# Performance work log

Hardware: AMD Instinct MI355X
Metric: run time of the kernel (lower is better)

Reference implementation:

```python
import jax, jax.numpy as jnp
import numpy as np

B, T, D, H = 8, 4096, 1024, 16
DK = D // H
CHUNK = 64
E, TOPK, MULT, CAPF = 8, 2, 4, 1.25
HID = D * MULT
N = B * T
CAPACITY = int(CAPF * (N / E))  # 5120


def setup_inputs() -> dict:
    key = jax.random.key(0)
    ks = jax.random.split(key, 16)
    s = 0.02
    r = lambda k, shape: jax.random.normal(k, shape, jnp.float32) * s
    return {
        "x": jax.random.normal(ks[0], (B, T, D), jnp.float32),
        "norm1_scale": jnp.ones((D,), jnp.float32),
        "norm2_scale": jnp.ones((D,), jnp.float32),
        "Wq": r(ks[1], (D, D)), "bq": jnp.zeros((D,), jnp.float32),
        "Wk": r(ks[2], (D, D)), "bk": jnp.zeros((D,), jnp.float32),
        "Wv": r(ks[3], (D, D)), "bv": jnp.zeros((D,), jnp.float32),
        "Wg": r(ks[4], (D, D)), "bg": jnp.zeros((D,), jnp.float32),
        "Wo": r(ks[5], (D, D)), "bo": jnp.zeros((D,), jnp.float32),
        "router_W": r(ks[6], (D, E)), "router_b": jnp.zeros((E,), jnp.float32),
        "W1": r(ks[7], (E, D, HID)), "b1": jnp.zeros((E, HID), jnp.float32),
        "W2": r(ks[8], (E, HID, D)), "b2": jnp.zeros((E, D), jnp.float32),
    }


def rmsnorm(x, scale):
    # torch: x / (||x|| / sqrt(d)) * scale == x * rsqrt(mean(x^2)) * scale (no eps)
    return x / jnp.sqrt(jnp.mean(x * x, axis=-1, keepdims=True)) * scale


def apply_rope(x):
    # x: (B, H, T, DK); non-interleaved half-rotation as in source
    half = x.shape[-1] // 2
    t = x.shape[2]
    inv = 1.0 / (10000.0 ** (jnp.arange(half, dtype=jnp.float32) / half))
    ang = jnp.arange(t, dtype=jnp.float32)[:, None] * inv[None, :]  # (T, half)
    sin, cos = jnp.sin(ang)[None, None], jnp.cos(ang)[None, None]
    x1, x2 = x[..., :half], x[..., half:]
    return jnp.concatenate([x1 * cos - x2 * sin, x1 * sin + x2 * cos], axis=-1)


def phi(x):
    return jax.nn.elu(x) + 1.0


def attention(x, Wq, bq, Wk, bk, Wv, bv, Wg, bg, Wo, bo):
    b, t, c = x.shape
    heads = lambda y: y.reshape(b, t, H, DK).transpose(0, 2, 1, 3)  # (B,H,T,DK)
    q = phi(apply_rope(heads(x @ Wq + bq)))
    k = phi(apply_rope(heads(x @ Wk + bk)))
    v = heads(x @ Wv + bv)
    g = heads(jax.nn.sigmoid(x @ Wg + bg))
    nc = t // CHUNK
    to_chunks = lambda y: y.reshape(b, H, nc, CHUNK, DK).transpose(2, 0, 1, 3, 4)
    qs, ks_, vs, gs = map(to_chunks, (q, k, v, g))  # (nc,B,H,chunk,DK)
    S0 = jnp.zeros((b, H, DK, DK), x.dtype)
    Z0 = jnp.zeros((b, H, DK), x.dtype)

    def step(carry, inp):
        S, Z = carry
        qc, kc, vc, gc = inp
        S = S + jnp.einsum('bhtd,bhte->bhde', kc, vc)
        Z = Z + kc.sum(axis=2)
        num = jnp.einsum('bhtd,bhde->bhte', qc, S)
        den = jnp.einsum('bhtd,bhd->bht', qc, Z)[..., None] + 1e-6
        return (S, Z), gc * (num / den)

    _, outs = jax.lax.scan(step, (S0, Z0), (qs, ks_, vs, gs))  # (nc,B,H,chunk,DK)
    out = outs.transpose(1, 2, 0, 3, 4).reshape(b, H, t, DK)
    out = out.transpose(0, 2, 1, 3).reshape(b, t, c)
    return out @ Wo + bo


def moe(x, router_W, router_b, W1, b1, W2, b2):
    b, t, c = x.shape
    n = b * t
    xf = x.reshape(n, c)
    probs = jax.nn.softmax(xf @ router_W + router_b, axis=-1)
    topk_probs, topk_idx = jax.lax.top_k(probs, TOPK)
    topk_probs = topk_probs / topk_probs.sum(axis=-1, keepdims=True)
    out = jnp.zeros_like(xf)
    load = []
    for eid in range(E):  # fixed small expert loop (matches source structure)
        mask = (topk_idx == eid).reshape(-1)  # row-major == torch.where order
        idx = jnp.nonzero(mask, size=CAPACITY, fill_value=n * TOPK)[0]
        valid = idx < n * TOPK
        idxc = jnp.minimum(idx, n * TOPK - 1)
        tok, choice = idxc // TOPK, idxc % TOPK
        h = jax.nn.gelu(xf[tok] @ W1[eid] + b1[eid], approximate=False) @ W2[eid] + b2[eid]
        gate = jnp.where(valid, topk_probs[tok, choice], 0.0)
        out = out.at[tok].add(gate[:, None] * h)  # invalid slots have gate==0
        load.append(jnp.minimum(mask.sum(), CAPACITY).astype(xf.dtype))
    load = jnp.stack(load)
    importance = probs.sum(axis=0)
    importance = importance / importance.sum()
    load = load / load.sum()
    aux = (importance * load).sum() * (E ** 2)
    return out.reshape(b, t, c), aux


def reference(x, norm1_scale, norm2_scale, Wq, bq, Wk, bk, Wv, bv, Wg, bg, Wo, bo,
              router_W, router_b, W1, b1, W2, b2):
    x = x + attention(rmsnorm(x, norm1_scale), Wq, bq, Wk, bk, Wv, bv, Wg, bg, Wo, bo)
    moe_out, aux = moe(rmsnorm(x, norm2_scale), router_W, router_b, W1, b1, W2, b2)
    return (x + moe_out, aux)
```

## Files before the change

### kernel.cpp

```cpp
#include <hip/hip_runtime.h>
#include <hip/hip_bf16.h>

#define NTOK 32768
#define TSEQ 4096
#define DM   1024
#define NHEAD 16
#define NEXP 8
#define CAPE 5120
#define HIDN 4096
#define GTOK 8192
#define KSPL 5120

#ifndef __has_builtin
#define __has_builtin(x) 0
#endif
#if __has_builtin(__builtin_amdgcn_global_load_lds)
#define HAVE_GLOAD 1
#else
#define HAVE_GLOAD 0
#endif

typedef __attribute__((ext_vector_type(8))) short bf16x8;
typedef __attribute__((ext_vector_type(4))) float f32x4;

__device__ __forceinline__ float phi_f(float v) { return v > 0.f ? v + 1.f : expf(v); }

__device__ __forceinline__ unsigned short f2bf_bits(float f) {
    __hip_bfloat16 h = __float2bfloat16(f);
    union { __hip_bfloat16 h; unsigned short s; } u;
    u.h = h;
    return u.s;
}
__device__ __forceinline__ float bf_to_f(unsigned short s) {
    unsigned int u = ((unsigned int)s) << 16;
    union { unsigned int u; float f; } w; w.u = u;
    return w.f;
}

__global__ void k_ws_flag(float* out, float v) { if (threadIdx.x == 0) out[0] = v; }

__global__ void k_zero(int* p, int n) {
    int i = blockIdx.x * 256 + threadIdx.x;
    if (i < n) p[i] = 0;
}

__global__ __launch_bounds__(256) void k_rope_table(float* __restrict__ ct, float* __restrict__ st)
{
    const int idx = blockIdx.x * 256 + threadIdx.x;
    const int t = idx >> 5, j = idx & 31;
    const float inv = (float)(1.0 / pow(10000.0, (double)j / 32.0));
    float sn, cn;
    sincosf((float)t * inv, &sn, &cn);
    ct[idx] = cn; st[idx] = sn;
}

struct WPack { const float* W[5]; };
__global__ __launch_bounds__(256) void k_build_wstack(WPack P, __hip_bfloat16* __restrict__ BTbase)
{
    __shared__ float t_[32][33];
    const int z = blockIdx.z;
    const float* Wm = P.W[z];
    __hip_bfloat16* BT = BTbase + (size_t)z * DM * KSPL;
    const int n0 = blockIdx.x * 32, k0 = blockIdx.y * 32;
    const int c = threadIdx.x & 31, r0 = (threadIdx.x >> 5);
#pragma unroll
    for (int i = 0; i < 4; ++i) { int r = r0 + i * 8; t_[r][c] = Wm[(size_t)(k0 + r) * DM + n0 + c]; }
    __syncthreads();
#pragma unroll
    for (int i = 0; i < 4; ++i) {
        int r = r0 + i * 8;
        float val = t_[c][r];
        unsigned short b0 = f2bf_bits(val);
        float res = val - bf_to_f(b0);
        unsigned short b1 = f2bf_bits(res);
        __hip_bfloat16 h0, h1;
        union { __hip_bfloat16 h; unsigned short s; } u0, u1;
        u0.s = b0; u1.s = b1; h0 = u0.h; h1 = u1.h;
        const size_t nrow = (size_t)(n0 + r) * KSPL + (k0 + c);
        BT[nrow]            = h0;
        BT[nrow + 1024]     = h0;
        BT[nrow + 2048]     = h0;
        BT[nrow + 3072]     = h1;
        BT[nrow + 4096]     = h1;
    }
}

template<bool NORM>
__global__ __launch_bounds__(256) void k_rms_split(const float* __restrict__ X,
                                                   const float* __restrict__ nscale,
                                                   __hip_bfloat16* __restrict__ Xs)
{
    const int row = blockIdx.x;
    const int tid = threadIdx.x;
    const float* xr = X + (size_t)row * DM;
    float4 v = ((const float4*)xr)[tid];
    float r = 1.f;
    if (NORM) {
        float s = v.x * v.x + v.y * v.y + v.z * v.z + v.w * v.w;
        for (int off = 32; off; off >>= 1) s += __shfl_xor(s, off);
        __shared__ float redw[4];
        __shared__ float rbc;
        if ((tid & 63) == 0) redw[tid >> 6] = s;
        __syncthreads();
        if (tid == 0) {
            float tot = redw[0] + redw[1] + redw[2] + redw[3];
            rbc = (float)(1.0 / sqrt((double)tot * (1.0 / 1024.0)));
        }
        __syncthreads();
        r = rbc;
    }
    float c[4] = {v.x, v.y, v.z, v.w};
    if (NORM) {
        float4 ns = ((const float4*)nscale)[tid];
        c[0] *= r * ns.x; c[1] *= r * ns.y; c[2] *= r * ns.z; c[3] *= r * ns.w;
    }
    ushort4 p0, p1, p2;
    unsigned short* q0 = (unsigned short*)&p0;
    unsigned short* q1 = (unsigned short*)&p1;
    unsigned short* q2 = (unsigned short*)&p2;
#pragma unroll
    for (int i = 0; i < 4; ++i) {
        float x = c[i];
        unsigned short b0 = f2bf_bits(x);
        float r1 = x - bf_to_f(b0);
        unsigned short b1 = f2bf_bits(r1);
        float r2 = r1 - bf_to_f(b1);
        unsigned short b2 = f2bf_bits(r2);
        q0[i] = b0; q1[i] = b1; q2[i] = b2;
    }
    __hip_bfloat16* base = Xs + (size_t)row * 3072;
    ((ushort4*)(base))[tid] = p0;
    ((ushort4*)(base + 1024))[tid] = p1;
    ((ushort4*)(base + 2048))[tid] = p2;
}

__global__ __launch_bounds__(256) void k_rmsnorm_stats(const float* __restrict__ X,
                                                       float* __restrict__ rn,
                                                       const float* __restrict__ nscale,
                                                       __hip_bfloat16* __restrict__ xbf)
{
    const int row = blockIdx.x;
    const int tid = threadIdx.x;
    const float* xr = X + (size_t)row * DM;
    float4 v = ((const float4*)xr)[tid];
    float s = v.x * v.x + v.y * v.y + v.z * v.z + v.w * v.w;
    for (int off = 32; off; off >>= 1) s += __shfl_xor(s, off);
    __shared__ float redw[4];
    __shared__ float rbc;
    if ((tid & 63) == 0) redw[tid >> 6] = s;
    __syncthreads();
    if (tid == 0) {
        float tot = redw[0] + redw[1] + redw[2] + redw[3];
        float r = (float)(1.0 / sqrt((double)tot * (1.0 / 1024.0)));
        rn[row] = r; rbc = r;
    }
    __syncthreads();
    float r = rbc;
    float4 ns = ((const float4*)nscale)[tid];
    ushort4 o;
    o.x = f2bf_bits(v.x * r * ns.x);
    o.y = f2bf_bits(v.y * r * ns.y);
    o.z = f2bf_bits(v.z * r * ns.z);
    o.w = f2bf_bits(v.w * r * ns.w);
    ((ushort4*)(xbf + (size_t)row * DM))[tid] = o;
}

#if HAVE_GLOAD
__device__ __forceinline__ void gload16(const __hip_bfloat16* g, __hip_bfloat16* l)
{
    __builtin_amdgcn_global_load_lds((const __attribute__((address_space(1))) unsigned int*)g,
                                     (__attribute__((address_space(3))) unsigned int*)l, 16, 0, 0);
}
#endif


struct ProjPack {
    const __hip_bfloat16* BT[4];
    const float* bias[4];
    float* C[4];
};

template<int NMAT, bool RESID>
__global__ __launch_bounds__(256) void k_gemm_proj(const __hip_bfloat16* __restrict__ A,
                                                   ProjPack P,
                                                   const float* __restrict__ resid)
{
    const int z = (NMAT == 4) ? blockIdx.z : 0;
    const __hip_bfloat16* BT = P.BT[z];
    const float* bias = P.bias[z];
    float* C = P.C[z];
    const int m0 = blockIdx.y * 128;
    const int n0 = blockIdx.x * 128;
    const int tid = threadIdx.x;
    __shared__ alignas(16) __hip_bfloat16 As[2][128 * 32];
    __shared__ alignas(16) __hip_bfloat16 Bs[2][128 * 32];

    const int lane = tid & 63, wv = tid >> 6;
    const int lr = lane & 15, lgp = lane >> 4;
    const int wm = (wv >> 1) * 64, wn = (wv & 1) * 64;

#if HAVE_GLOAD
    const int rA0 = wv * 32 + (lane >> 2), rA1 = rA0 + 16;
    const int ch = lane & 3;
    const __hip_bfloat16* srcA0 = A + (size_t)(m0 + rA0) * 3072 + ((ch ^ (rA0 & 3)) * 8);
    const __hip_bfloat16* srcA1 = A + (size_t)(m0 + rA1) * 3072 + ((ch ^ (rA1 & 3)) * 8);
    const __hip_bfloat16* srcB0 = BT + (size_t)(n0 + rA0) * KSPL + ((ch ^ (rA0 & 3)) * 8);
    const __hip_bfloat16* srcB1 = BT + (size_t)(n0 + rA1) * KSPL + ((ch ^ (rA1 & 3)) * 8);
    const int ldsO0 = (wv * 32) * 32;
    const int ldsO1 = (wv * 32 + 16) * 32;
#else
    const int ar = tid >> 1, ac0 = (tid & 1) * 2;
    const __hip_bfloat16* Arow = A + (size_t)(m0 + ar) * 3072;
    const __hip_bfloat16* Brow = BT + (size_t)(n0 + ar) * KSPL;
#endif

    f32x4 acc[4][4];
#pragma unroll
    for (int i = 0; i < 4; ++i)
#pragma unroll
        for (int j = 0; j < 4; ++j) acc[i][j] = (f32x4){0.f, 0.f, 0.f, 0.f};

    int a_off[4], b_off[4];
#pragma unroll
    for (int i = 0; i < 4; ++i) {
        int mrow = wm + i * 16 + lr;
        a_off[i] = mrow * 32 + ((lgp ^ (mrow & 3)) * 8);
        int nrow = wn + i * 16 + lr;
        b_off[i] = nrow * 32 + ((lgp ^ (nrow & 3)) * 8);
    }

#if HAVE_GLOAD
    gload16(srcA0, &As[0][ldsO0]);
    gload16(srcA1, &As[0][ldsO1]);
    gload16(srcB0, &Bs[0][ldsO0]);
    gload16(srcB1, &Bs[0][ldsO1]);
#else
    {
        uint4 av0 = *(const uint4*)(Arow + ac0 * 8);
        uint4 av1 = *(const uint4*)(Arow + ac0 * 8 + 8);
        uint4 bv0 = *(const uint4*)(Brow + ac0 * 8);
        uint4 bv1 = *(const uint4*)(Brow + ac0 * 8 + 8);
        *(uint4*)(&As[0][0] + ar * 32 + ((ac0    ) ^ (ar & 3)) * 8) = av0;
        *(uint4*)(&As[0][0] + ar * 32 + ((ac0 + 1) ^ (ar & 3)) * 8) = av1;
        *(uint4*)(&Bs[0][0] + ar * 32 + ((ac0    ) ^ (ar & 3)) * 8) = bv0;
        *(uint4*)(&Bs[0][0] + ar * 32 + ((ac0 + 1) ^ (ar & 3)) * 8) = bv1;
    }
#endif
    __syncthreads();

    int cur = 0;
    for (int k0 = 0; k0 < KSPL; k0 += 32) {
        if (k0 + 32 < KSPL) {
            const int kn = k0 + 32;
            const int acoln = (kn < 3072) ? kn : (kn - 3072);
#if HAVE_GLOAD
            gload16(srcA0 + acoln, &As[cur ^ 1][ldsO0]);
            gload16(srcA1 + acoln, &As[cur ^ 1][ldsO1]);
            gload16(srcB0 + kn, &Bs[cur ^ 1][ldsO0]);
            gload16(srcB1 + kn, &Bs[cur ^ 1][ldsO1]);
#else
            uint4 av0 = *(const uint4*)(Arow + acoln + ac0 * 8);
            uint4 av1 = *(const uint4*)(Arow + acoln + ac0 * 8 + 8);
            uint4 bv0 = *(const uint4*)(Brow + kn + ac0 * 8);
            uint4 bv1 = *(const uint4*)(Brow + kn + ac0 * 8 + 8);
            *(uint4*)(&As[cur ^ 1][0] + ar * 32 + ((ac0    ) ^ (ar & 3)) * 8) = av0;
            *(uint4*)(&As[cur ^ 1][0] + ar * 32 + ((ac0 + 1) ^ (ar & 3)) * 8) = av1;
            *(uint4*)(&Bs[cur ^ 1][0] + ar * 32 + ((ac0    ) ^ (ar & 3)) * 8) = bv0;
            *(uint4*)(&Bs[cur ^ 1][0] + ar * 32 + ((ac0 + 1) ^ (ar & 3)) * 8) = bv1;
#endif
        }
        bf16x8 af[4], bfr[4];
#pragma unroll
        for (int i = 0; i < 4; ++i) af[i] = *(const bf16x8*)(&As[cur][0] + a_off[i]);
#pragma unroll
        for (int j = 0; j < 4; ++j) bfr[j] = *(const bf16x8*)(&Bs[cur][0] + b_off[j]);
#pragma unroll
        for (int i = 0; i < 4; ++i)
#pragma unroll
            for (int j = 0; j < 4; ++j)
                acc[i][j] = __builtin_amdgcn_mfma_f32_16x16x32_bf16(af[i], bfr[j], acc[i][j], 0, 0, 0);
        __syncthreads();
        cur ^= 1;
    }

#pragma unroll
    for (int i = 0; i < 4; ++i)
#pragma unroll
        for (int j = 0; j < 4; ++j) {
            const int col = n0 + wn + j * 16 + lr;
            const float bval = bias[col];
#pragma unroll
            for (int r = 0; r < 4; ++r) {
                const int rloc = wm + i * 16 + lgp * 4 + r;
                float v = acc[i][j][r] + bval;
                if (RESID) v += resid[(size_t)(m0 + rloc) * DM + col];
                C[(size_t)(m0 + rloc) * DM + col] = v;
            }
        }
}

template<int MODE>
__global__ __launch_bounds__(256) void k_gemm_bf16(const __hip_bfloat16* __restrict__ A,
                                                   const __hip_bfloat16* __restrict__ BT,
                                                   const float* __restrict__ bias,
                                                   __hip_bfloat16* __restrict__ Hout,
                                                   float* __restrict__ Fout,
                                                   const int* __restrict__ tokslot,
                                                   const float* __restrict__ gateslot,
                                                   int K, int Nout, int e0)
{
    const int le = blockIdx.z;
    const int e = e0 + le;
    const int m0 = blockIdx.y * 128;
    const int n0 = blockIdx.x * 128;
    const int tid = threadIdx.x;
    __shared__ alignas(16) __hip_bfloat16 As[2][128 * 32];
    __shared__ alignas(16) __hip_bfloat16 Bs[2][128 * 32];
    __shared__ int s_tok[128];
    __shared__ float s_gate[128];
    if (tid < 128) {
        s_tok[tid] = tokslot[e * CAPE + m0 + tid];
        s_gate[tid] = gateslot[e * CAPE + m0 + tid];
    }
    __syncthreads();

    const int lane = tid & 63, wv = tid >> 6;
    const int lr = lane & 15, lgp = lane >> 4;
    const int wm = (wv >> 1) * 64, wn = (wv & 1) * 64;

#if HAVE_GLOAD
    const int rA0 = wv * 32 + (lane >> 2), rA1 = rA0 + 16;
    const int ch = lane & 3;
    const __hip_bfloat16 *srcA0, *srcA1;
    if (MODE == 0) {
        srcA0 = A + (size_t)s_tok[rA0] * K + ((ch ^ (rA0 & 3)) * 8);
        srcA1 = A + (size_t)s_tok[rA1] * K + ((ch ^ (rA1 & 3)) * 8);
    } else {
        srcA0 = A + ((size_t)le * CAPE + m0 + rA0) * K + ((ch ^ (rA0 & 3)) * 8);
        srcA1 = A + ((size_t)le * CAPE + m0 + rA1) * K + ((ch ^ (rA1 & 3)) * 8);
    }
    const __hip_bfloat16* srcB0 = BT + ((size_t)e * Nout + n0 + rA0) * K + ((ch ^ (rA0 & 3)) * 8);
    const __hip_bfloat16* srcB1 = BT + ((size_t)e * Nout + n0 + rA1) * K + ((ch ^ (rA1 & 3)) * 8);
    const int ldsO0 = (wv * 32) * 32;
    const int ldsO1 = (wv * 32 + 16) * 32;
#else
    const int ar = tid >> 1, ac0 = (tid & 1) * 2;
    const __hip_bfloat16* Arow;
    if (MODE == 0) Arow = A + (size_t)s_tok[ar] * K;
    else           Arow = A + ((size_t)le * CAPE + m0 + ar) * K;
    const __hip_bfloat16* Brow = BT + ((size_t)e * Nout + n0 + ar) * K;
#endif

    f32x4 acc[4][4];
#pragma unroll
    for (int i = 0; i < 4; ++i)
#pragma unroll
        for (int j = 0; j < 4; ++j) acc[i][j] = (f32x4){0.f, 0.f, 0.f, 0.f};

    int a_off[4], b_off[4];
#pragma unroll
    for (int i = 0; i < 4; ++i) {
        int mrow = wm + i * 16 + lr;
        a_off[i] = mrow * 32 + ((lgp ^ (mrow & 3)) * 8);
        int nrow = wn + i * 16 + lr;
        b_off[i] = nrow * 32 + ((lgp ^ (nrow & 3)) * 8);
    }

#if HAVE_GLOAD
    gload16(srcA0, &As[0][ldsO0]);
    gload16(srcA1, &As[0][ldsO1]);
    gload16(srcB0, &Bs[0][ldsO0]);
    gload16(srcB1, &Bs[0][ldsO1]);
#else
    {
        uint4 av0 = *(const uint4*)(Arow + ac0 * 8);
        uint4 av1 = *(const uint4*)(Arow + ac0 * 8 + 8);
        uint4 bv0 = *(const uint4*)(Brow + ac0 * 8);
        uint4 bv1 = *(const uint4*)(Brow + ac0 * 8 + 8);
        *(uint4*)(&As[0][0] + ar * 32 + ((ac0    ) ^ (ar & 3)) * 8) = av0;
        *(uint4*)(&As[0][0] + ar * 32 + ((ac0 + 1) ^ (ar & 3)) * 8) = av1;
        *(uint4*)(&Bs[0][0] + ar * 32 + ((ac0    ) ^ (ar & 3)) * 8) = bv0;
        *(uint4*)(&Bs[0][0] + ar * 32 + ((ac0 + 1) ^ (ar & 3)) * 8) = bv1;
    }
#endif
    __syncthreads();

    int cur = 0;
    for (int k0 = 0; k0 < K; k0 += 32) {
        if (k0 + 32 < K) {
            const int kn = k0 + 32;
#if HAVE_GLOAD
            gload16(srcA0 + kn, &As[cur ^ 1][ldsO0]);
            gload16(srcA1 + kn, &As[cur ^ 1][ldsO1]);
            gload16(srcB0 + kn, &Bs[cur ^ 1][ldsO0]);
            gload16(srcB1 + kn, &Bs[cur ^ 1][ldsO1]);
#else
            uint4 av0 = *(const uint4*)(Arow + kn + ac0 * 8);
            uint4 av1 = *(const uint4*)(Arow + kn + ac0 * 8 + 8);
            uint4 bv0 = *(const uint4*)(Brow + kn + ac0 * 8);
            uint4 bv1 = *(const uint4*)(Brow + kn + ac0 * 8 + 8);
            *(uint4*)(&As[cur ^ 1][0] + ar * 32 + ((ac0    ) ^ (ar & 3)) * 8) = av0;
            *(uint4*)(&As[cur ^ 1][0] + ar * 32 + ((ac0 + 1) ^ (ar & 3)) * 8) = av1;
            *(uint4*)(&Bs[cur ^ 1][0] + ar * 32 + ((ac0    ) ^ (ar & 3)) * 8) = bv0;
            *(uint4*)(&Bs[cur ^ 1][0] + ar * 32 + ((ac0 + 1) ^ (ar & 3)) * 8) = bv1;
#endif
        }
        bf16x8 af[4], bfr[4];
#pragma unroll
        for (int i = 0; i < 4; ++i) af[i] = *(const bf16x8*)(&As[cur][0] + a_off[i]);
#pragma unroll
        for (int j = 0; j < 4; ++j) bfr[j] = *(const bf16x8*)(&Bs[cur][0] + b_off[j]);
#pragma unroll
        for (int i = 0; i < 4; ++i)
#pragma unroll
            for (int j = 0; j < 4; ++j)
                acc[i][j] = __builtin_amdgcn_mfma_f32_16x16x32_bf16(af[i], bfr[j], acc[i][j], 0, 0, 0);
        __syncthreads();
        cur ^= 1;
    }

#pragma unroll
    for (int i = 0; i < 4; ++i)
#pragma unroll
        for (int j = 0; j < 4; ++j) {
            const int col = n0 + wn + j * 16 + lr;
            const float bval = bias[(size_t)e * Nout + col];
#pragma unroll
            for (int r = 0; r < 4; ++r) {
                const int rloc = wm + i * 16 + lgp * 4 + r;
                float v = acc[i][j][r] + bval;
                if (MODE == 0) {
                    v = 0.5f * v * (1.f + erff(v * 0.70710678118654752f));
                    Hout[((size_t)le * CAPE + m0 + rloc) * Nout + col] = __float2bfloat16(v);
                } else {
                    const float g = s_gate[rloc];
                    if (g != 0.f) atomicAdd(&Fout[(size_t)s_tok[rloc] * DM + col], v * g);
                }
            }
        }
}

__global__ __launch_bounds__(256) void k_scan_kv(float* KS, float* Vz,
                                                 const float* __restrict__ ct,
                                                 const float* __restrict__ st)
{
    const int c = blockIdx.x, bh = blockIdx.y;
    const int h = bh & 15, b = bh >> 4;
    const int tid = threadIdx.x;
    __shared__ float ks[64][68];
    __shared__ float vs[64][68];
    const size_t rowbase = ((size_t)b * TSEQ + c * 64) * DM + h * 64;
#pragma unroll
    for (int p = 0; p < 8; ++p) {
        int idx = p * 256 + tid;
        int t = idx >> 5, j = idx & 31;
        const size_t base = rowbase + (size_t)t * DM + j;
        float cn = ct[(c * 64 + t) * 32 + j];
        float sn = st[(c * 64 + t) * 32 + j];
        float k1 = KS[base], k2 = KS[base + 32];
        ks[t][j]      = phi_f(k1 * cn - k2 * sn);
        ks[t][j + 32] = phi_f(k1 * sn + k2 * cn);
    }
#pragma unroll
    for (int p = 0; p < 4; ++p) {
        int idx = p * 256 + tid;
        int t = idx >> 4, e4 = (idx & 15) * 4;
        *(float4*)&vs[t][e4] = *(const float4*)&Vz[rowbase + (size_t)t * DM + e4];
    }
    __syncthreads();
    const int e = tid & 63, dg = tid >> 6;
    float acc[16] = {};
    for (int t = 0; t < 64; ++t) {
        float vv = vs[t][e];
#pragma unroll
        for (int qq = 0; qq < 4; ++qq) {
            float4 kq = *(const float4*)&ks[t][dg * 16 + qq * 4];
            acc[qq * 4 + 0] = fmaf(kq.x, vv, acc[qq * 4 + 0]);
            acc[qq * 4 + 1] = fmaf(kq.y, vv, acc[qq * 4 + 1]);
            acc[qq * 4 + 2] = fmaf(kq.z, vv, acc[qq * 4 + 2]);
            acc[qq * 4 + 3] = fmaf(kq.w, vv, acc[qq * 4 + 3]);
        }
    }
#pragma unroll
    for (int i = 0; i < 16; ++i) {
        int d = dg * 16 + i;
        KS[rowbase + (size_t)d * DM + e] = acc[i];
    }
    if (tid < 64) {
        float z = 0.f;
        for (int t = 0; t < 64; ++t) z += ks[t][tid];
        Vz[rowbase + tid] = z;
    }
}

__global__ __launch_bounds__(256) void k_scan_prefix(float* S)
{
    const int sg = blockIdx.x, bh = blockIdx.y;
    const int h = bh & 15, b = bh >> 4;
    const int idx = sg * 256 + threadIdx.x;
    const int d = idx >> 6, e = idx & 63;
    const size_t base = (size_t)b * TSEQ * DM + h * 64 + (size_t)d * DM + e;
    float acc = 0.f;
    for (int c = 0; c < 64; ++c) {
        size_t p = base + (size_t)c * 64 * DM;
        acc += S[p];
        S[p] = acc;
    }
}

__global__ void k_zprefix(float* Vz)
{
    const int bh = blockIdx.x;
    const int h = bh & 15, b = bh >> 4;
    const int d = threadIdx.x;
    const size_t base = (size_t)b * TSEQ * DM + h * 64 + d;
    float acc = 0.f;
    for (int c = 0; c < 64; ++c) {
        size_t p = base + (size_t)c * 64 * DM;
        acc += Vz[p];
        Vz[p] = acc;
    }
}

__global__ __launch_bounds__(256) void k_scan_out(const float* __restrict__ Q,
                                                  const float* __restrict__ S,
                                                  const float* __restrict__ Zv,
                                                  const float* __restrict__ G,
                                                  __hip_bfloat16* __restrict__ Xs,
                                                  const float* __restrict__ ct,
                                                  const float* __restrict__ st)
{
    const int c = blockIdx.x, bh = blockIdx.y;
    const int h = bh & 15, b = bh >> 4;
    const int tid = threadIdx.x;
    __shared__ float qs[64][69];
    __shared__ float Ss[64][68];
    __shared__ float den[64], Zl[64];
    const size_t rowbase = ((size_t)b * TSEQ + c * 64) * DM + h * 64;
#pragma unroll
    for (int p = 0; p < 8; ++p) {
        int idx = p * 256 + tid;
        int t = idx >> 5, j = idx & 31;
        const size_t base = rowbase + (size_t)t * DM + j;
        float cn = ct[(c * 64 + t) * 32 + j];
        float sn = st[(c * 64 + t) * 32 + j];
        float q1 = Q[base], q2 = Q[base + 32];
        qs[t][j]      = phi_f(q1 * cn - q2 * sn);
        qs[t][j + 32] = phi_f(q1 * sn + q2 * cn);
    }
#pragma unroll
    for (int p = 0; p < 4; ++p) {
        int idx = p * 256 + tid;
        int d = idx >> 4, e4 = (idx & 15) * 4;
        *(float4*)&Ss[d][e4] = *(const float4*)&S[rowbase + (size_t)d * DM + e4];
    }
    const int e = tid & 63, tg = tid >> 6;
    float greg[16];
#pragma unroll
    for (int i = 0; i < 16; ++i)
        greg[i] = G[rowbase + (size_t)(tg * 16 + i) * DM + e];
    if (tid < 64) Zl[tid] = Zv[rowbase + tid];
    __syncthreads();
    if (tid < 64) {
        float dd = 0.f;
        for (int d = 0; d < 64; ++d) dd += qs[tid][d] * Zl[d];
        den[tid] = dd + 1e-6f;
    }
    __syncthreads();
    float acc[16] = {};
    for (int d = 0; d < 64; ++d) {
        float sv = Ss[d][e];
#pragma unroll
        for (int i = 0; i < 16; ++i)
            acc[i] = fmaf(qs[tg * 16 + i][d], sv, acc[i]);
    }
    unsigned short* Xu = (unsigned short*)Xs;
#pragma unroll
    for (int i = 0; i < 16; ++i) {
        int t = tg * 16 + i;
        float g = 1.f / (1.f + expf(-greg[i]));
        float o = g * acc[i] / den[t];
        unsigned short b0 = f2bf_bits(o);
        float r1 = o - bf_to_f(b0);
        unsigned short b1 = f2bf_bits(r1);
        float r2 = r1 - bf_to_f(b1);
        unsigned short b2 = f2bf_bits(r2);
        const size_t xb = (size_t)(b * TSEQ + c * 64 + t) * 3072 + h * 64 + e;
        Xu[xb] = b0;
        Xu[xb + 1024] = b1;
        Xu[xb + 2048] = b2;
    }
}

__global__ __launch_bounds__(256) void k_router(const float* __restrict__ X2,
                                                const float* __restrict__ rn2,
                                                const float* __restrict__ ns2,
                                                const float* __restrict__ rW,
                                                const float* __restrict__ rb,
                                                int* __restrict__ route_e,
                                                float* __restrict__ route_g,
                                                float* __restrict__ probs)
{
    const int tok = blockIdx.x * 4 + (threadIdx.x >> 6);
    const int lane = threadIdx.x & 63;
    const float* xr = X2 + (size_t)tok * DM;
    const float rn = rn2[tok];
    float lg[8] = {};
    for (int d = lane; d < DM; d += 64) {
        float xv = xr[d] * rn * ns2[d];
        const float4* w4 = (const float4*)(rW + (size_t)d * 8);
        float4 w0 = w4[0], w1 = w4[1];
        lg[0] += xv * w0.x; lg[1] += xv * w0.y; lg[2] += xv * w0.z; lg[3] += xv * w0.w;
        lg[4] += xv * w1.x; lg[5] += xv * w1.y; lg[6] += xv * w1.z; lg[7] += xv * w1.w;
    }
#pragma unroll
    for (int e = 0; e < 8; ++e)
        for (int off = 32; off; off >>= 1) lg[e] += __shfl_xor(lg[e], off);
    if (lane == 0) {
        float pe[8]; float mx = -1e30f, s = 0.f;
#pragma unroll
        for (int e = 0; e < 8; ++e) { lg[e] += rb[e]; mx = fmaxf(mx, lg[e]); }
#pragma unroll
        for (int e = 0; e < 8; ++e) { pe[e] = expf(lg[e] - mx); s += pe[e]; }
#pragma unroll
        for (int e = 0; e < 8; ++e) { pe[e] /= s; probs[(size_t)tok * 8 + e] = pe[e]; }
        int i1 = 0; float p1 = pe[0];
#pragma unroll
        for (int e = 1; e < 8; ++e) if (pe[e] > p1) { p1 = pe[e]; i1 = e; }
        int i2 = -1; float p2 = -1.f;
#pragma unroll
        for (int e = 0; e < 8; ++e) if (e != i1 && pe[e] > p2) { p2 = pe[e]; i2 = e; }
        const float gsum = p1 + p2;
        route_e[tok * 2] = i1; route_e[tok * 2 + 1] = i2;
        route_g[tok * 2] = p1 / gsum; route_g[tok * 2 + 1] = p2 / gsum;
    }
}

__global__ __launch_bounds__(256) void k_count(const int* __restrict__ route_e, int* __restrict__ bcnt)
{
    __shared__ int c[8];
    const int tid = threadIdx.x;
    if (tid < 8) c[tid] = 0;
    __syncthreads();
    atomicAdd(&c[route_e[blockIdx.x * 256 + tid]], 1);
    __syncthreads();
    if (tid < 8) bcnt[blockIdx.x * 8 + tid] = c[tid];
}

__global__ void k_scan_blocks(const int* __restrict__ bcnt, int* __restrict__ bbase, int* __restrict__ ctot)
{
    const int e = threadIdx.x;
    if (e < 8) {
        int run = 0;
        for (int b = 0; b < 256; ++b) { bbase[b * 8 + e] = run; run += bcnt[b * 8 + e]; }
        ctot[e] = run;
    }
}

__global__ __launch_bounds__(256) void k_place(const int* __restrict__ route_e,
                                               const float* __restrict__ route_g,
                                               const int* __restrict__ bbase,
                                               int* __restrict__ tokslot,
                                               float* __restrict__ gateslot)
{
    const int tid = threadIdx.x;
    const int a = blockIdx.x * 256 + tid;
    const int e = route_e[a];
    __shared__ int se[256];
    se[tid] = e;
    __syncthreads();
    int rank = 0;
    for (int j = 0; j < tid; ++j) rank += (se[j] == e) ? 1 : 0;
    const int slot = bbase[blockIdx.x * 8 + e] + rank;
    if (slot < CAPE) {
        tokslot[e * CAPE + slot] = a >> 1;
        gateslot[e * CAPE + slot] = route_g[a];
    }
}

__global__ __launch_bounds__(256) void k_aux(const float* __restrict__ probs,
                                             const int* __restrict__ ctot,
                                             float* __restrict__ out_aux)
{
    const int tid = threadIdx.x;
    float part[8] = {};
    for (int i = tid; i < NTOK; i += 256) {
        const float* p = probs + (size_t)i * 8;
#pragma unroll
        for (int e = 0; e < 8; ++e) part[e] += p[e];
    }
    __shared__ float red[256];
    __shared__ float accs[8];
    for (int e = 0; e < 8; ++e) {
        red[tid] = part[e];
        __syncthreads();
        for (int s = 128; s; s >>= 1) { if (tid < s) red[tid] += red[tid + s]; __syncthreads(); }
        if (tid == 0) accs[e] = red[0];
        __syncthreads();
    }
    if (tid == 0) {
        float isum = 0.f, lsum = 0.f, l[8];
        for (int e = 0; e < 8; ++e) isum += accs[e];
        for (int e = 0; e < 8; ++e) { l[e] = fminf((float)ctot[e], (float)CAPE); lsum += l[e]; }
        float aux = 0.f;
        for (int e = 0; e < 8; ++e) aux += (accs[e] / isum) * (l[e] / lsum);
        out_aux[0] = aux * 64.f;
    }
}

__global__ void k_transpose_bf16(const float* __restrict__ src, __hip_bfloat16* __restrict__ dst,
                                 int K_, int N_)
{
    __shared__ float t_[32][33];
    const int z = blockIdx.z;
    const float* s = src + (size_t)z * K_ * N_;
    __hip_bfloat16* d = dst + (size_t)z * K_ * N_;
    const int n0 = blockIdx.x * 32, k0 = blockIdx.y * 32;
    const int c = threadIdx.x, r0 = threadIdx.y;
#pragma unroll
    for (int i = 0; i < 4; ++i) { int r = r0 + i * 8; t_[r][c] = s[(size_t)(k0 + r) * N_ + n0 + c]; }
    __syncthreads();
#pragma unroll
    for (int i = 0; i < 4; ++i) { int r = r0 + i * 8; d[(size_t)(n0 + r) * K_ + k0 + c] = __float2bfloat16(t_[c][r]); }
}

extern "C" void kernel_launch(void* const* d_in, const int* in_sizes, int n_in,
                              void* d_out, int out_size, void* d_ws, size_t ws_size,
                              hipStream_t stream)
{
    (void)in_sizes; (void)n_in; (void)out_size;
    const float* x   = (const float*)d_in[0];
    const float* ns1 = (const float*)d_in[1];
    const float* ns2 = (const float*)d_in[2];
    const float* Wq  = (const float*)d_in[3];
    const float* bq  = (const float*)d_in[4];
    const float* Wk  = (const float*)d_in[5];
    const float* bk  = (const float*)d_in[6];
    const float* Wv  = (const float*)d_in[7];
    const float* bv  = (const float*)d_in[8];
    const float* Wg  = (const float*)d_in[9];
    const float* bg  = (const float*)d_in[10];
    const float* Wo  = (const float*)d_in[11];
    const float* bo  = (const float*)d_in[12];
    const float* rW  = (const float*)d_in[13];
    const float* rb  = (const float*)d_in[14];
    const float* W1  = (const float*)d_in[15];
    const float* b1  = (const float*)d_in[16];
    const float* W2  = (const float*)d_in[17];
    const float* b2  = (const float*)d_in[18];
    float* out = (float*)d_out;
    char* wsb = (char*)d_ws;

    constexpr size_t MiB = 1024ull * 1024ull;
    constexpr size_t R = (size_t)NTOK * DM * 4;
    constexpr size_t TAIL = 3 * R;
    constexpr size_t OFF_RN1  = TAIL;
    constexpr size_t OFF_RN2  = OFF_RN1 + (size_t)NTOK * 4;
    constexpr size_t OFF_PROB = OFF_RN2 + (size_t)NTOK * 4;
    constexpr size_t OFF_RE   = OFF_PROB + (size_t)NTOK * 8 * 4;
    constexpr size_t OFF_RG   = OFF_RE + (size_t)NTOK * 2 * 4;
    constexpr size_t OFF_BCNT = OFF_RG + (size_t)NTOK * 2 * 4;
    constexpr size_t OFF_BBASE= OFF_BCNT + 256 * 8 * 4;
    constexpr size_t OFF_CTOT = OFF_BBASE + 256 * 8 * 4;
    constexpr size_t OFF_TOK  = OFF_CTOT + 4096;
    constexpr size_t OFF_GATE = OFF_TOK + (size_t)NEXP * CAPE * 4;
    constexpr size_t REQUIRED = OFF_GATE + (size_t)NEXP * CAPE * 4;

    if (ws_size < REQUIRED) {
        k_ws_flag<<<1, 64, 0, stream>>>(out, (float)(ws_size >> 20));
        return;
    }

    __hip_bfloat16* xn2bf = (__hip_bfloat16*)(wsb);
    __hip_bfloat16* WST   = (__hip_bfloat16*)(wsb + 64 * MiB);
    __hip_bfloat16* Xs    = (__hip_bfloat16*)(wsb + 114 * MiB);
    float* qg = (float*)(wsb + 162 * MiB);
    float* kg = (float*)(wsb + 194 * MiB);
    float* gg = (float*)(wsb + 226 * MiB);
    __hip_bfloat16* W1T  = (__hip_bfloat16*)(wsb + 64 * MiB);
    __hip_bfloat16* W2T  = (__hip_bfloat16*)(wsb + 128 * MiB);
    __hip_bfloat16* Hbuf = (__hip_bfloat16*)(wsb + 192 * MiB);

    float* rn2 = (float*)(wsb + OFF_RN2);
    float* probs = (float*)(wsb + OFF_PROB);
    float* rope_ct = (float*)(wsb + OFF_PROB);
    float* rope_st = (float*)(wsb + OFF_PROB + (size_t)TSEQ * 32 * 4);
    int*   route_e = (int*)(wsb + OFF_RE);
    float* route_g = (float*)(wsb + OFF_RG);
    int*   bcnt  = (int*)(wsb + OFF_BCNT);
    int*   bbase = (int*)(wsb + OFF_BBASE);
    int*   ctot  = (int*)(wsb + OFF_CTOT);
    int*   tokslot  = (int*)(wsb + OFF_TOK);
    float* gateslot = (float*)(wsb + OFF_GATE);

    k_rope_table<<<512, 256, 0, stream>>>(rope_ct, rope_st);
    {
        WPack WP; WP.W[0] = Wq; WP.W[1] = Wk; WP.W[2] = Wg; WP.W[3] = Wv; WP.W[4] = Wo;
        k_build_wstack<<<dim3(32, 32, 5), 256, 0, stream>>>(WP, WST);
    }

    for (int gi = 0; gi < 4; ++gi) {
        const size_t tok0 = (size_t)gi * GTOK;
        const float* xg = x + tok0 * DM;
        float* vg = out + tok0 * DM;

        k_rms_split<true><<<GTOK, 256, 0, stream>>>(xg, ns1, Xs);

        ProjPack P;
        P.BT[0] = WST;                     P.bias[0] = bq; P.C[0] = qg;
        P.BT[1] = WST + (size_t)DM * KSPL; P.bias[1] = bk; P.C[1] = kg;
        P.BT[2] = WST + 2ull * DM * KSPL;  P.bias[2] = bg; P.C[2] = gg;
        P.BT[3] = WST + 3ull * DM * KSPL;  P.bias[3] = bv; P.C[3] = vg;
        k_gemm_proj<4, false><<<dim3(8, GTOK / 128, 4), 256, 0, stream>>>(Xs, P, nullptr);

        k_scan_kv<<<dim3(64, 32), 256, 0, stream>>>(kg, vg, rope_ct, rope_st);
        k_scan_prefix<<<dim3(16, 32), 256, 0, stream>>>(kg);
        k_zprefix<<<32, 64, 0, stream>>>(vg);
        k_scan_out<<<dim3(64, 32), 256, 0, stream>>>(qg, kg, vg, gg, Xs, rope_ct, rope_st);

        ProjPack P2;
        P2.BT[0] = WST + 4ull * DM * KSPL; P2.bias[0] = bo; P2.C[0] = vg;
        P2.BT[1] = P2.BT[2] = P2.BT[3] = P2.BT[0];
        P2.bias[1] = P2.bias[2] = P2.bias[3] = bo;
        P2.C[1] = P2.C[2] = P2.C[3] = vg;
        k_gemm_proj<1, true><<<dim3(8, GTOK / 128, 1), 256, 0, stream>>>(Xs, P2, xg);

        k_rmsnorm_stats<<<GTOK, 256, 0, stream>>>(vg, rn2 + tok0, ns2, xn2bf + tok0 * DM);
    }

    k_router<<<NTOK / 4, 256, 0, stream>>>(out, rn2, ns2, rW, rb, route_e, route_g, probs);

    k_count<<<256, 256, 0, stream>>>(route_e, bcnt);
    k_scan_blocks<<<1, 64, 0, stream>>>(bcnt, bbase, ctot);
    k_zero<<<(NEXP * CAPE * 2 + 255) / 256, 256, 0, stream>>>(tokslot, NEXP * CAPE * 2);
    k_place<<<256, 256, 0, stream>>>(route_e, route_g, bbase, tokslot, gateslot);

    k_aux<<<1, 256, 0, stream>>>(probs, ctot, out + (size_t)NTOK * DM);

    k_transpose_bf16<<<dim3(HIDN / 32, DM / 32, NEXP), dim3(32, 8), 0, stream>>>(W1, W1T, DM, HIDN);
    k_transpose_bf16<<<dim3(DM / 32, HIDN / 32, NEXP), dim3(32, 8), 0, stream>>>(W2, W2T, HIDN, DM);

    for (int g = 0; g < 3; ++g) {
        const int e0 = g * 3;
        const int ecnt = (g == 2) ? 2 : 3;
        k_gemm_bf16<0><<<dim3(HIDN / 128, CAPE / 128, ecnt), 256, 0, stream>>>(
            xn2bf, W1T, b1, Hbuf, nullptr, tokslot, gateslot, DM, HIDN, e0);
        k_gemm_bf16<1><<<dim3(DM / 128, CAPE / 128, ecnt), 256, 0, stream>>>(
            Hbuf, W2T, b2, nullptr, out, tokslot, gateslot, HIDN, DM, e0);
    }
}
```

Before: 4.610 ms.

## Use triple-buffered LDS pipeline with explicit vmcnt waits in GEMM kernels

The projection and expert GEMM kernels move from a double-buffered LDS scheme to a three-stage ring. Three tiles are prefetched through global_load_lds, and the loop waits with explicit s_waitcnt vmcnt counts and raw s_barrier calls instead of __syncthreads. This lets the loads for tile t+3 overlap the MFMA work on tile t and takes the blanket vmcnt(0) out of each iteration. In exchange LDS use per block rises by half, which may lower occupancy, and correctness now depends on the hand-written wait counts matching the number of outstanding loads.

```diff
diff --git a/kernel.cpp b/kernel.cpp
--- a/kernel.cpp
+++ b/kernel.cpp
@@ -22,6 +22,11 @@
 
 typedef __attribute__((ext_vector_type(8))) short bf16x8;
 typedef __attribute__((ext_vector_type(4))) float f32x4;
+
+#define WAITCNT8() asm volatile("s_waitcnt vmcnt(8)" ::: "memory")
+#define WAITCNT4() asm volatile("s_waitcnt vmcnt(4)" ::: "memory")
+#define WAITCNT0() asm volatile("s_waitcnt vmcnt(0)" ::: "memory")
+#define RAWBAR()   do { asm volatile("" ::: "memory"); __builtin_amdgcn_s_barrier(); asm volatile("" ::: "memory"); } while (0)
 
 __device__ __forceinline__ float phi_f(float v) { return v > 0.f ? v + 1.f : expf(v); }
 
@@ -192,12 +197,29 @@
     const int m0 = blockIdx.y * 128;
     const int n0 = blockIdx.x * 128;
     const int tid = threadIdx.x;
-    __shared__ alignas(16) __hip_bfloat16 As[2][128 * 32];
-    __shared__ alignas(16) __hip_bfloat16 Bs[2][128 * 32];
+    __shared__ alignas(16) __hip_bfloat16 As[3][128 * 32];
+    __shared__ alignas(16) __hip_bfloat16 Bs[3][128 * 32];
 
     const int lane = tid & 63, wv = tid >> 6;
     const int lr = lane & 15, lgp = lane >> 4;
     const int wm = (wv >> 1) * 64, wn = (wv & 1) * 64;
+
+    f32x4 acc[4][4];
+#pragma unroll
+    for (int i = 0; i < 4; ++i)
+#pragma unroll
+        for (int j = 0; j < 4; ++j) acc[i][j] = (f32x4){0.f, 0.f, 0.f, 0.f};
+
+    int a_off[4], b_off[4];
+#pragma unroll
+    for (int i = 0; i < 4; ++i) {
+        int mrow = wm + i * 16 + lr;
+        a_off[i] = mrow * 32 + ((lgp ^ (mrow & 3)) * 8);
+        int nrow = wn + i * 16 + lr;
+        b_off[i] = nrow * 32 + ((lgp ^ (nrow & 3)) * 8);
+    }
+
+    constexpr int T = KSPL / 32;
 
 #if HAVE_GLOAD
     const int rA0 = wv * 32 + (lane >> 2), rA1 = rA0 + 16;
@@ -208,80 +230,68 @@
     const __hip_bfloat16* srcB1 = BT + (size_t)(n0 + rA1) * KSPL + ((ch ^ (rA1 & 3)) * 8);
     const int ldsO0 = (wv * 32) * 32;
     const int ldsO1 = (wv * 32 + 16) * 32;
+
+    auto STAGE = [&](int tile, int buf) {
+        const int kb = tile * 32;
+        const int acol = (kb < 3072) ? kb : (kb - 3072);
+        gload16(srcA0 + acol, &As[buf][ldsO0]);
+        gload16(srcA1 + acol, &As[buf][ldsO1]);
+        gload16(srcB0 + kb,  &Bs[buf][ldsO0]);
+        gload16(srcB1 + kb,  &Bs[buf][ldsO1]);
+    };
+
+    STAGE(0, 0); STAGE(1, 1); STAGE(2, 2);
+    int buf = 0;
+    for (int t = 0; t < T; ++t) {
+        if (t <= T - 3)      { WAITCNT8(); }
+        else if (t == T - 2) { WAITCNT4(); }
+        else                 { WAITCNT0(); }
+        RAWBAR();
+        bf16x8 af[4], bfr[4];
+#pragma unroll
+        for (int i = 0; i < 4; ++i) af[i] = *(const bf16x8*)(&As[buf][0] + a_off[i]);
+#pragma unroll
+        for (int j = 0; j < 4; ++j) bfr[j] = *(const bf16x8*)(&Bs[buf][0] + b_off[j]);
+#pragma unroll
+        for (int i = 0; i < 4; ++i)
+#pragma unroll
+            for (int j = 0; j < 4; ++j)
+                acc[i][j] = __builtin_amdgcn_mfma_f32_16x16x32_bf16(af[i], bfr[j], acc[i][j], 0, 0, 0);
+        if (t + 3 < T) {
+            RAWBAR();
+            STAGE(t + 3, buf);
+        }
+        buf = (buf == 2) ? 0 : buf + 1;
+    }
 #else
     const int ar = tid >> 1, ac0 = (tid & 1) * 2;
     const __hip_bfloat16* Arow = A + (size_t)(m0 + ar) * 3072;
     const __hip_bfloat16* Brow = BT + (size_t)(n0 + ar) * KSPL;
-#endif
-
-    f32x4 acc[4][4];
-#pragma unroll
-    for (int i = 0; i < 4; ++i)
-#pragma unroll
-        for (int j = 0; j < 4; ++j) acc[i][j] = (f32x4){0.f, 0.f, 0.f, 0.f};
-
-    int a_off[4], b_off[4];
-#pragma unroll
-    for (int i = 0; i < 4; ++i) {
-        int mrow = wm + i * 16 + lr;
-        a_off[i] = mrow * 32 + ((lgp ^ (mrow & 3)) * 8);
-        int nrow = wn + i * 16 + lr;
-        b_off[i] = nrow * 32 + ((lgp ^ (nrow & 3)) * 8);
-    }
-
-#if HAVE_GLOAD
-    gload16(srcA0, &As[0][ldsO0]);
-    gload16(srcA1, &As[0][ldsO1]);
-    gload16(srcB0, &Bs[0][ldsO0]);
-    gload16(srcB1, &Bs[0][ldsO1]);
-#else
-    {
-        uint4 av0 = *(const uint4*)(Arow + ac0 * 8);
-        uint4 av1 = *(const uint4*)(Arow + ac0 * 8 + 8);
-        uint4 bv0 = *(const uint4*)(Brow + ac0 * 8);
-        uint4 bv1 = *(const uint4*)(Brow + ac0 * 8 + 8);
+    for (int t = 0; t < T; ++t) {
+        const int kb = t * 32;
+        const int acol = (kb < 3072) ? kb : (kb - 3072);
+        __syncthreads();
+        uint4 av0 = *(const uint4*)(Arow + acol + ac0 * 8);
+        uint4 av1 = *(const uint4*)(Arow + acol + ac0 * 8 + 8);
+        uint4 bv0 = *(const uint4*)(Brow + kb + ac0 * 8);
+        uint4 bv1 = *(const uint4*)(Brow + kb + ac0 * 8 + 8);
         *(uint4*)(&As[0][0] + ar * 32 + ((ac0    ) ^ (ar & 3)) * 8) = av0;
         *(uint4*)(&As[0][0] + ar * 32 + ((ac0 + 1) ^ (ar & 3)) * 8) = av1;
         *(uint4*)(&Bs[0][0] + ar * 32 + ((ac0    ) ^ (ar & 3)) * 8) = bv0;
         *(uint4*)(&Bs[0][0] + ar * 32 + ((ac0 + 1) ^ (ar & 3)) * 8) = bv1;
-    }
-#endif
-    __syncthreads();
-
-    int cur = 0;
-    for (int k0 = 0; k0 < KSPL; k0 += 32) {
-        if (k0 + 32 < KSPL) {
-            const int kn = k0 + 32;
-            const int acoln = (kn < 3072) ? kn : (kn - 3072);
-#if HAVE_GLOAD
-            gload16(srcA0 + acoln, &As[cur ^ 1][ldsO0]);
-            gload16(srcA1 + acoln, &As[cur ^ 1][ldsO1]);
-            gload16(srcB0 + kn, &Bs[cur ^ 1][ldsO0]);
-            gload16(srcB1 + kn, &Bs[cur ^ 1][ldsO1]);
-#else
-            uint4 av0 = *(const uint4*)(Arow + acoln + ac0 * 8);
-            uint4 av1 = *(const uint4*)(Arow + acoln + ac0 * 8 + 8);
-            uint4 bv0 = *(const uint4*)(Brow + kn + ac0 * 8);
-            uint4 bv1 = *(const uint4*)(Brow + kn + ac0 * 8 + 8);
-            *(uint4*)(&As[cur ^ 1][0] + ar * 32 + ((ac0    ) ^ (ar & 3)) * 8) = av0;
-            *(uint4*)(&As[cur ^ 1][0] + ar * 32 + ((ac0 + 1) ^ (ar & 3)) * 8) = av1;
-            *(uint4*)(&Bs[cur ^ 1][0] + ar * 32 + ((ac0    ) ^ (ar & 3)) * 8) = bv0;
-            *(uint4*)(&Bs[cur ^ 1][0] + ar * 32 + ((ac0 + 1) ^ (ar & 3)) * 8) = bv1;
-#endif
-        }
+        __syncthreads();
         bf16x8 af[4], bfr[4];
 #pragma unroll
-        for (int i = 0; i < 4; ++i) af[i] = *(const bf16x8*)(&As[cur][0] + a_off[i]);
-#pragma unroll
-        for (int j = 0; j < 4; ++j) bfr[j] = *(const bf16x8*)(&Bs[cur][0] + b_off[j]);
+        for (int i = 0; i < 4; ++i) af[i] = *(const bf16x8*)(&As[0][0] + a_off[i]);
+#pragma unroll
+        for (int j = 0; j < 4; ++j) bfr[j] = *(const bf16x8*)(&Bs[0][0] + b_off[j]);
 #pragma unroll
         for (int i = 0; i < 4; ++i)
 #pragma unroll
             for (int j = 0; j < 4; ++j)
                 acc[i][j] = __builtin_amdgcn_mfma_f32_16x16x32_bf16(af[i], bfr[j], acc[i][j], 0, 0, 0);
-        __syncthreads();
-        cur ^= 1;
-    }
+    }
+#endif
 
 #pragma unroll
     for (int i = 0; i < 4; ++i)
@@ -314,8 +324,8 @@
     const int m0 = blockIdx.y * 128;
     const int n0 = blockIdx.x * 128;
     const int tid = threadIdx.x;
-    __shared__ alignas(16) __hip_bfloat16 As[2][128 * 32];
-    __shared__ alignas(16) __hip_bfloat16 Bs[2][128 * 32];
+    __shared__ alignas(16) __hip_bfloat16 As[3][128 * 32];
+    __shared__ alignas(16) __hip_bfloat16 Bs[3][128 * 32];
     __shared__ int s_tok[128];
     __shared__ float s_gate[128];
     if (tid < 128) {
@@ -327,6 +337,21 @@
     const int lane = tid & 63, wv = tid >> 6;
     const int lr = lane & 15, lgp = lane >> 4;
     const int wm = (wv >> 1) * 64, wn = (wv & 1) * 64;
+
+    f32x4 acc[4][4];
+#pragma unroll
+    for (int i = 0; i < 4; ++i)
+#pragma unroll
+        for (int j = 0; j < 4; ++j) acc[i][j] = (f32x4){0.f, 0.f, 0.f, 0.f};
+
+    int a_off[4], b_off[4];
+#pragma unroll
+    for (int i = 0; i < 4; ++i) {
+        int mrow = wm + i * 16 + lr;
+        a_off[i] = mrow * 32 + ((lgp ^ (mrow & 3)) * 8);
+        int nrow = wn + i * 16 + lr;
+        b_off[i] = nrow * 32 + ((lgp ^ (nrow & 3)) * 8);
+    }
 
 #if HAVE_GLOAD
     const int rA0 = wv * 32 + (lane >> 2), rA1 = rA0 + 16;
@@ -343,81 +368,68 @@
     const __hip_bfloat16* srcB1 = BT + ((size_t)e * Nout + n0 + rA1) * K + ((ch ^ (rA1 & 3)) * 8);
     const int ldsO0 = (wv * 32) * 32;
     const int ldsO1 = (wv * 32 + 16) * 32;
+
+    auto STAGE = [&](int tile, int buf) {
+        const int kb = tile * 32;
+        gload16(srcA0 + kb, &As[buf][ldsO0]);
+        gload16(srcA1 + kb, &As[buf][ldsO1]);
+        gload16(srcB0 + kb, &Bs[buf][ldsO0]);
+        gload16(srcB1 + kb, &Bs[buf][ldsO1]);
+    };
+
+    const int T = K / 32;
+    STAGE(0, 0); STAGE(1, 1); STAGE(2, 2);
+    int buf = 0;
+    for (int t = 0; t < T; ++t) {
+        if (t <= T - 3)      { WAITCNT8(); }
+        else if (t == T - 2) { WAITCNT4(); }
+        else                 { WAITCNT0(); }
+        RAWBAR();
+        bf16x8 af[4], bfr[4];
+#pragma unroll
+        for (int i = 0; i < 4; ++i) af[i] = *(const bf16x8*)(&As[buf][0] + a_off[i]);
+#pragma unroll
+        for (int j = 0; j < 4; ++j) bfr[j] = *(const bf16x8*)(&Bs[buf][0] + b_off[j]);
+#pragma unroll
+        for (int i = 0; i < 4; ++i)
+#pragma unroll
+            for (int j = 0; j < 4; ++j)
+                acc[i][j] = __builtin_amdgcn_mfma_f32_16x16x32_bf16(af[i], bfr[j], acc[i][j], 0, 0, 0);
+        if (t + 3 < T) {
+            RAWBAR();
+            STAGE(t + 3, buf);
+        }
+        buf = (buf == 2) ? 0 : buf + 1;
+    }
 #else
     const int ar = tid >> 1, ac0 = (tid & 1) * 2;
     const __hip_bfloat16* Arow;
     if (MODE == 0) Arow = A + (size_t)s_tok[ar] * K;
     else           Arow = A + ((size_t)le * CAPE + m0 + ar) * K;
     const __hip_bfloat16* Brow = BT + ((size_t)e * Nout + n0 + ar) * K;
-#endif
-
-    f32x4 acc[4][4];
-#pragma unroll
-    for (int i = 0; i < 4; ++i)
-#pragma unroll
-        for (int j = 0; j < 4; ++j) acc[i][j] = (f32x4){0.f, 0.f, 0.f, 0.f};
-
-    int a_off[4], b_off[4];
-#pragma unroll
-    for (int i = 0; i < 4; ++i) {
-        int mrow = wm + i * 16 + lr;
-        a_off[i] = mrow * 32 + ((lgp ^ (mrow & 3)) * 8);
-        int nrow = wn + i * 16 + lr;
-        b_off[i] = nrow * 32 + ((lgp ^ (nrow & 3)) * 8);
-    }
-
-#if HAVE_GLOAD
-    gload16(srcA0, &As[0][ldsO0]);
-    gload16(srcA1, &As[0][ldsO1]);
-    gload16(srcB0, &Bs[0][ldsO0]);
-    gload16(srcB1, &Bs[0][ldsO1]);
-#else
-    {
-        uint4 av0 = *(const uint4*)(Arow + ac0 * 8);
-        uint4 av1 = *(const uint4*)(Arow + ac0 * 8 + 8);
-        uint4 bv0 = *(const uint4*)(Brow + ac0 * 8);
-        uint4 bv1 = *(const uint4*)(Brow + ac0 * 8 + 8);
+    for (int k0 = 0; k0 < K; k0 += 32) {
+        __syncthreads();
+        uint4 av0 = *(const uint4*)(Arow + k0 + ac0 * 8);
+        uint4 av1 = *(const uint4*)(Arow + k0 + ac0 * 8 + 8);
+        uint4 bv0 = *(const uint4*)(Brow + k0 + ac0 * 8);
+        uint4 bv1 = *(const uint4*)(Brow + k0 + ac0 * 8 + 8);
         *(uint4*)(&As[0][0] + ar * 32 + ((ac0    ) ^ (ar & 3)) * 8) = av0;
         *(uint4*)(&As[0][0] + ar * 32 + ((ac0 + 1) ^ (ar & 3)) * 8) = av1;
         *(uint4*)(&Bs[0][0] + ar * 32 + ((ac0    ) ^ (ar & 3)) * 8) = bv0;
         *(uint4*)(&Bs[0][0] + ar * 32 + ((ac0 + 1) ^ (ar & 3)) * 8) = bv1;
-    }
-#endif
-    __syncthreads();
-
-    int cur = 0;
-    for (int k0 = 0; k0 < K; k0 += 32) {
-        if (k0 + 32 < K) {
-            const int kn = k0 + 32;
-#if HAVE_GLOAD
-            gload16(srcA0 + kn, &As[cur ^ 1][ldsO0]);
-            gload16(srcA1 + kn, &As[cur ^ 1][ldsO1]);
-            gload16(srcB0 + kn, &Bs[cur ^ 1][ldsO0]);
-            gload16(srcB1 + kn, &Bs[cur ^ 1][ldsO1]);
-#else
-            uint4 av0 = *(const uint4*)(Arow + kn + ac0 * 8);
-            uint4 av1 = *(const uint4*)(Arow + kn + ac0 * 8 + 8);
-            uint4 bv0 = *(const uint4*)(Brow + kn + ac0 * 8);
-            uint4 bv1 = *(const uint4*)(Brow + kn + ac0 * 8 + 8);
-            *(uint4*)(&As[cur ^ 1][0] + ar * 32 + ((ac0    ) ^ (ar & 3)) * 8) = av0;
-            *(uint4*)(&As[cur ^ 1][0] + ar * 32 + ((ac0 + 1) ^ (ar & 3)) * 8) = av1;
-            *(uint4*)(&Bs[cur ^ 1][0] + ar * 32 + ((ac0    ) ^ (ar & 3)) * 8) = bv0;
-            *(uint4*)(&Bs[cur ^ 1][0] + ar * 32 + ((ac0 + 1) ^ (ar & 3)) * 8) = bv1;
-#endif
-        }
+        __syncthreads();
         bf16x8 af[4], bfr[4];
 #pragma unroll
-        for (int i = 0; i < 4; ++i) af[i] = *(const bf16x8*)(&As[cur][0] + a_off[i]);
-#pragma unroll
-        for (int j = 0; j < 4; ++j) bfr[j] = *(const bf16x8*)(&Bs[cur][0] + b_off[j]);
+        for (int i = 0; i < 4; ++i) af[i] = *(const bf16x8*)(&As[0][0] + a_off[i]);
+#pragma unroll
+        for (int j = 0; j < 4; ++j) bfr[j] = *(const bf16x8*)(&Bs[0][0] + b_off[j]);
 #pragma unroll
         for (int i = 0; i < 4; ++i)
 #pragma unroll
             for (int j = 0; j < 4; ++j)
                 acc[i][j] = __builtin_amdgcn_mfma_f32_16x16x32_bf16(af[i], bfr[j], acc[i][j], 0, 0, 0);
-        __syncthreads();
-        cur ^= 1;
-    }
+    }
+#endif
 
 #pragma unroll
     for (int i = 0; i < 4; ++i)
```

Result: faster. 4.508 ms (-2.2%).
